# Kernel optimization log

Measured on AMD Instinct MI355X. Metric: run time of the kernel, lower is better.

Reference implementation:

```python
import jax, jax.numpy as jnp
import numpy as np

WIN_SIZE = 256
PATCH_SIZE = [8]
CHANNEL = 32
B_CH = 256        # B_outer(8) * CHANNEL(32)
H, E = 8, 64


def _attn(q, k):
    # q, k: [B*ch, L, H, E] -> softmax scores [B*ch, H, L, L]
    scale = 1.0 / jnp.sqrt(jnp.asarray(E, q.dtype))
    scores = jnp.einsum('blhe,bshe->bhls', q, k) * scale
    return jax.nn.softmax(scores, axis=-1)  # dropout is identity in eval


def _channel_mean(a):
    # '(b reduce_b) l m n -> b l m n' mean with reduce_b=CHANNEL (channel innermost)
    bc, h, m, n = a.shape
    return a.reshape(bc // CHANNEL, CHANNEL, h, m, n).mean(axis=1)


def setup_inputs() -> dict:
    key = jax.random.key(0)
    k1, k2, k3, k4 = jax.random.split(key, 4)
    p = PATCH_SIZE[0]
    patch_num = WIN_SIZE // p
    return {
        'queries_patch_size': jax.random.normal(k1, (B_CH, patch_num, H, E), jnp.float32),
        'keys_patch_size':    jax.random.normal(k2, (B_CH, patch_num, H, E), jnp.float32),
        'queries_patch_num':  jax.random.normal(k3, (B_CH, p, H, E), jnp.float32),
        'keys_patch_num':     jax.random.normal(k4, (B_CH, p, H, E), jnp.float32),
        'patch_index': 0,
        'attn_mask': 0,
    }


def reference(queries_patch_size, keys_patch_size, queries_patch_num, keys_patch_num, patch_index, attn_mask):
    p = PATCH_SIZE[patch_index]
    rep = WIN_SIZE // p

    # patch_size branch: element-wise repeat (einops repeat) then channel mean.
    # mean over channel commutes with the repeat, so reduce first (same math,
    # avoids the 536MB intermediate the torch code materializes).
    s_ps = _channel_mean(_attn(queries_patch_size, keys_patch_size))  # [B,H,rep,rep]
    s_ps = jnp.repeat(jnp.repeat(s_ps, p, axis=2), p, axis=3)

    # patch_num branch: torch .repeat == tile, then channel mean (also commutes).
    s_pn = _channel_mean(_attn(queries_patch_num, keys_patch_num))    # [B,H,p,p]
    s_pn = jnp.tile(s_pn, (1, 1, rep, rep))

    return (s_ps, s_pn)
```

## Files before the change

### kernel.cpp

```cpp
#include <hip/hip_runtime.h>
#include <stdint.h>


__global__ __launch_bounds__(256)
void scores_kernel(const float* __restrict__ qps,
                   const float* __restrict__ kps,
                   const float* __restrict__ qpn,
                   const float* __restrict__ kpn,
                   float* __restrict__ ws_ps,
                   float* __restrict__ ws_pn)
{
    __shared__ float red[4][32 * 36];
    const int tid  = threadIdx.x;
    const int wv   = tid >> 6;
    const int lane = tid & 63;
    const int blk  = blockIdx.x;

    if (blk < 512) {
        const int a     = blk >> 3;
        const int chunk = blk & 7;
        const int bo = a >> 3, h = a & 7;
        const int ch = chunk * 4 + wv;
        const int b  = bo * 32 + ch;
        const int i = lane >> 3, j = lane & 7;

        const float4* Q = reinterpret_cast<const float4*>(qps) + ((b * 32 + 4 * i) * 8 + h) * 16;
        const float4* K = reinterpret_cast<const float4*>(kps) + ((b * 32 + 4 * j) * 8 + h) * 16;

        float acc[4][4];
        #pragma unroll
        for (int r = 0; r < 4; ++r)
            #pragma unroll
            for (int c = 0; c < 4; ++c) acc[r][c] = 0.f;

        #pragma unroll 4
        for (int c = 0; c < 16; ++c) {
            float4 q[4], k[4];
            #pragma unroll
            for (int r = 0; r < 4; ++r) { q[r] = Q[r * 128 + c]; k[r] = K[r * 128 + c]; }
            #pragma unroll
            for (int r = 0; r < 4; ++r)
                #pragma unroll
                for (int u = 0; u < 4; ++u) {
                    acc[r][u] = fmaf(q[r].x, k[u].x, acc[r][u]);
                    acc[r][u] = fmaf(q[r].y, k[u].y, acc[r][u]);
                    acc[r][u] = fmaf(q[r].z, k[u].z, acc[r][u]);
                    acc[r][u] = fmaf(q[r].w, k[u].w, acc[r][u]);
                }
        }

        #pragma unroll
        for (int r = 0; r < 4; ++r) {
            float v0 = acc[r][0] * 0.125f, v1 = acc[r][1] * 0.125f;
            float v2 = acc[r][2] * 0.125f, v3 = acc[r][3] * 0.125f;
            float m = fmaxf(fmaxf(v0, v1), fmaxf(v2, v3));
            m = fmaxf(m, __shfl_xor(m, 1));
            m = fmaxf(m, __shfl_xor(m, 2));
            m = fmaxf(m, __shfl_xor(m, 4));
            float e0 = __expf(v0 - m), e1 = __expf(v1 - m);
            float e2 = __expf(v2 - m), e3 = __expf(v3 - m);
            float s = (e0 + e1) + (e2 + e3);
            s += __shfl_xor(s, 1);
            s += __shfl_xor(s, 2);
            s += __shfl_xor(s, 4);
            const float inv = 1.f / (s * 32.f);
            float4 p; p.x = e0 * inv; p.y = e1 * inv; p.z = e2 * inv; p.w = e3 * inv;
            *reinterpret_cast<float4*>(&red[wv][(4 * i + r) * 36 + 4 * j]) = p;
        }
        __syncthreads();

        const int l = tid >> 3, s4 = (tid & 7) * 4;
        const float4 u0 = *reinterpret_cast<const float4*>(&red[0][l * 36 + s4]);
        const float4 u1 = *reinterpret_cast<const float4*>(&red[1][l * 36 + s4]);
        const float4 u2 = *reinterpret_cast<const float4*>(&red[2][l * 36 + s4]);
        const float4 u3 = *reinterpret_cast<const float4*>(&red[3][l * 36 + s4]);
        float4 o;
        o.x = (u0.x + u1.x) + (u2.x + u3.x);
        o.y = (u0.y + u1.y) + (u2.y + u3.y);
        o.z = (u0.z + u1.z) + (u2.z + u3.z);
        o.w = (u0.w + u1.w) + (u2.w + u3.w);
        reinterpret_cast<float4*>(ws_ps + (a * 8 + chunk) * 1024)[tid] = o;
    } else {
        const int bb    = blk - 512;
        const int a2    = bb >> 3;
        const int chunk = bb & 7;
        const int bo = a2 >> 3, h = a2 & 7;
        const int b  = bo * 32 + chunk * 4 + wv;
        const int i = lane >> 3, j = lane & 7;
        const float4* qv = reinterpret_cast<const float4*>(qpn) + ((b * 8 + i) * 8 + h) * 16;
        const float4* kv = reinterpret_cast<const float4*>(kpn) + ((b * 8 + j) * 8 + h) * 16;

        float acc = 0.f;
        #pragma unroll
        for (int c = 0; c < 16; ++c) {
            float4 q = qv[c], k = kv[c];
            acc = fmaf(q.x, k.x, acc);
            acc = fmaf(q.y, k.y, acc);
            acc = fmaf(q.z, k.z, acc);
            acc = fmaf(q.w, k.w, acc);
        }
        const float s = acc * 0.125f;
        float m = s;
        m = fmaxf(m, __shfl_xor(m, 1));
        m = fmaxf(m, __shfl_xor(m, 2));
        m = fmaxf(m, __shfl_xor(m, 4));
        float e = __expf(s - m);
        float sum = e;
        sum += __shfl_xor(sum, 1);
        sum += __shfl_xor(sum, 2);
        sum += __shfl_xor(sum, 4);

        red[wv][lane] = e / (sum * 32.f);
        __syncthreads();
        if (tid < 64) {
            ws_pn[(a2 * 8 + chunk) * 64 + tid] =
                (red[0][tid] + red[1][tid]) + (red[2][tid] + red[3][tid]);
        }
    }
}

__global__ __launch_bounds__(256)
void reduce_kernel(const float* __restrict__ ws_ps,
                   const float* __restrict__ ws_pn,
                   float* __restrict__ ws0r,
                   float* __restrict__ ws1r)
{
    const int g = blockIdx.x * 256 + threadIdx.x;
    if (g < 65536) {
        const int a = g >> 10, c = g & 1023;
        const float* base = ws_ps + a * 8192 + c;
        float v = 0.f;
        #pragma unroll
        for (int k = 0; k < 8; ++k) v += base[k * 1024];
        ws0r[g] = v;
    } else {
        const int h = g - 65536;
        const int a = h >> 6, c = h & 63;
        const float* base = ws_pn + a * 512 + c;
        float v = 0.f;
        #pragma unroll
        for (int k = 0; k < 8; ++k) v += base[k * 64];
        ws1r[h] = v;
    }
}

__global__ __launch_bounds__(256)
void writer_kernel(const float* __restrict__ ws0r,
                   const float* __restrict__ ws1r,
                   float* __restrict__ out)
{
    const int g = blockIdx.x * 256 + threadIdx.x;
    float4* o4 = reinterpret_cast<float4*>(out);
    if (g < 1048576) {
        const int a  = g >> 14;
        const int r  = g & 16383;
        const int i  = r >> 6;
        const int j4 = r & 63;
        const float v = ws0r[a * 1024 + (i >> 3) * 32 + (j4 >> 1)];
        float4 o; o.x = v; o.y = v; o.z = v; o.w = v;
        o4[g] = o;
    } else {
        const int g2 = g - 1048576;
        const int a  = g2 >> 14;
        const int r  = g2 & 16383;
        const int i  = r >> 6;
        const int j4 = r & 63;
        o4[g] = *reinterpret_cast<const float4*>(ws1r + a * 64 + (i & 7) * 8 + 4 * (j4 & 1));
    }
}

extern "C" void kernel_launch(void* const* d_in, const int* in_sizes, int n_in,
                              void* d_out, int out_size, void* d_ws, size_t ws_size,
                              hipStream_t stream) {
    const float *qps = nullptr, *kps = nullptr, *qpn = nullptr, *kpn = nullptr;
    for (int idx = 0; idx < n_in; ++idx) {
        if (in_sizes[idx] == 256 * 32 * 8 * 64) {
            if (!qps) qps = (const float*)d_in[idx];
            else if (!kps) kps = (const float*)d_in[idx];
        } else if (in_sizes[idx] == 256 * 8 * 8 * 64) {
            if (!qpn) qpn = (const float*)d_in[idx];
            else if (!kpn) kpn = (const float*)d_in[idx];
        }
    }

    float* ws_ps = (float*)d_ws;
    float* ws_pn = ws_ps + 64 * 8 * 1024;
    float* ws0r  = ws_pn + 64 * 8 * 64;
    float* ws1r  = ws0r + 64 * 1024;

    scores_kernel<<<1024, 256, 0, stream>>>(qps, kps, qpn, kpn, ws_ps, ws_pn);
    reduce_kernel<<<272, 256, 0, stream>>>(ws_ps, ws_pn, ws0r, ws1r);
    writer_kernel<<<8192, 256, 0, stream>>>(ws0r, ws1r, (float*)d_out);
}
```

Measured before the change: 118.6 us.

## Stage Q/K tiles in LDS with double buffering and per-thread channel accumulation

The patch_size branch now loads each channel's 32x64 Q and K tiles cooperatively into shared memory with coalesced float4 loads, double-buffered across the block's four channels. Each thread computes one row-group of scores per channel and accumulates the softmax output in registers, which removes the cross-wave LDS reduction. Before, each wave gathered strided global rows and issued redundant global loads across lanes. In exchange, channels inside a block are processed serially with a barrier per channel, and occupancy is pinned through launch_bounds.

Result: faster. 108.8 us (-8.3%).

```diff
diff --git a/kernel.cpp b/kernel.cpp
--- a/kernel.cpp
+++ b/kernel.cpp
@@ -2,7 +2,7 @@
 #include <stdint.h>
 
 
-__global__ __launch_bounds__(256)
+__global__ __launch_bounds__(256, 4)
 void scores_kernel(const float* __restrict__ qps,
                    const float* __restrict__ kps,
                    const float* __restrict__ qpn,
@@ -10,7 +10,7 @@
                    float* __restrict__ ws_ps,
                    float* __restrict__ ws_pn)
 {
-    __shared__ float red[4][32 * 36];
+    __shared__ float4 tiles[2][2][32 * 17];
     const int tid  = threadIdx.x;
     const int wv   = tid >> 6;
     const int lane = tid & 63;
@@ -20,67 +20,94 @@
         const int a     = blk >> 3;
         const int chunk = blk & 7;
         const int bo = a >> 3, h = a & 7;
-        const int ch = chunk * 4 + wv;
-        const int b  = bo * 32 + ch;
-        const int i = lane >> 3, j = lane & 7;
-
-        const float4* Q = reinterpret_cast<const float4*>(qps) + ((b * 32 + 4 * i) * 8 + h) * 16;
-        const float4* K = reinterpret_cast<const float4*>(kps) + ((b * 32 + 4 * j) * 8 + h) * 16;
-
-        float acc[4][4];
-        #pragma unroll
-        for (int r = 0; r < 4; ++r)
+        const int b0 = bo * 32 + chunk * 4;
+
+        const float4* Q4 = reinterpret_cast<const float4*>(qps);
+        const float4* K4 = reinterpret_cast<const float4*>(kps);
+
+        const int r0 = tid >> 4;
+        const int f  = tid & 15;
+
+        const int myrow = wv * 8 + (lane >> 3);
+        const int j     = lane & 7;
+
+        float pa[4];
+        #pragma unroll
+        for (int u = 0; u < 4; ++u) pa[u] = 0.f;
+
+        float4 gq0, gq1, gk0, gk1;
+        {
+            const int b = b0;
+            gq0 = Q4[((b * 32 + r0) * 8 + h) * 16 + f];
+            gq1 = Q4[((b * 32 + 16 + r0) * 8 + h) * 16 + f];
+            gk0 = K4[((b * 32 + r0) * 8 + h) * 16 + f];
+            gk1 = K4[((b * 32 + 16 + r0) * 8 + h) * 16 + f];
+            tiles[0][0][r0 * 17 + f]        = gq0;
+            tiles[0][0][(16 + r0) * 17 + f] = gq1;
+            tiles[0][1][r0 * 17 + f]        = gk0;
+            tiles[0][1][(16 + r0) * 17 + f] = gk1;
+        }
+        __syncthreads();
+
+        for (int ch = 0; ch < 4; ++ch) {
+            const int buf = ch & 1;
+
+            if (ch < 3) {
+                const int b = b0 + ch + 1;
+                gq0 = Q4[((b * 32 + r0) * 8 + h) * 16 + f];
+                gq1 = Q4[((b * 32 + 16 + r0) * 8 + h) * 16 + f];
+                gk0 = K4[((b * 32 + r0) * 8 + h) * 16 + f];
+                gk1 = K4[((b * 32 + 16 + r0) * 8 + h) * 16 + f];
+            }
+
+            float acc[4];
             #pragma unroll
-            for (int c = 0; c < 4; ++c) acc[r][c] = 0.f;
-
-        #pragma unroll 4
-        for (int c = 0; c < 16; ++c) {
-            float4 q[4], k[4];
+            for (int u = 0; u < 4; ++u) acc[u] = 0.f;
             #pragma unroll
-            for (int r = 0; r < 4; ++r) { q[r] = Q[r * 128 + c]; k[r] = K[r * 128 + c]; }
-            #pragma unroll
-            for (int r = 0; r < 4; ++r)
+            for (int c = 0; c < 16; ++c) {
+                const float4 q = tiles[buf][0][myrow * 17 + c];
                 #pragma unroll
                 for (int u = 0; u < 4; ++u) {
-                    acc[r][u] = fmaf(q[r].x, k[u].x, acc[r][u]);
-                    acc[r][u] = fmaf(q[r].y, k[u].y, acc[r][u]);
-                    acc[r][u] = fmaf(q[r].z, k[u].z, acc[r][u]);
-                    acc[r][u] = fmaf(q[r].w, k[u].w, acc[r][u]);
+                    const float4 k = tiles[buf][1][(4 * j + u) * 17 + c];
+                    acc[u] = fmaf(q.x, k.x, acc[u]);
+                    acc[u] = fmaf(q.y, k.y, acc[u]);
+                    acc[u] = fmaf(q.z, k.z, acc[u]);
+                    acc[u] = fmaf(q.w, k.w, acc[u]);
                 }
-        }
-
-        #pragma unroll
-        for (int r = 0; r < 4; ++r) {
-            float v0 = acc[r][0] * 0.125f, v1 = acc[r][1] * 0.125f;
-            float v2 = acc[r][2] * 0.125f, v3 = acc[r][3] * 0.125f;
-            float m = fmaxf(fmaxf(v0, v1), fmaxf(v2, v3));
-            m = fmaxf(m, __shfl_xor(m, 1));
-            m = fmaxf(m, __shfl_xor(m, 2));
-            m = fmaxf(m, __shfl_xor(m, 4));
-            float e0 = __expf(v0 - m), e1 = __expf(v1 - m);
-            float e2 = __expf(v2 - m), e3 = __expf(v3 - m);
-            float s = (e0 + e1) + (e2 + e3);
-            s += __shfl_xor(s, 1);
-            s += __shfl_xor(s, 2);
-            s += __shfl_xor(s, 4);
-            const float inv = 1.f / (s * 32.f);
-            float4 p; p.x = e0 * inv; p.y = e1 * inv; p.z = e2 * inv; p.w = e3 * inv;
-            *reinterpret_cast<float4*>(&red[wv][(4 * i + r) * 36 + 4 * j]) = p;
-        }
-        __syncthreads();
-
-        const int l = tid >> 3, s4 = (tid & 7) * 4;
-        const float4 u0 = *reinterpret_cast<const float4*>(&red[0][l * 36 + s4]);
-        const float4 u1 = *reinterpret_cast<const float4*>(&red[1][l * 36 + s4]);
-        const float4 u2 = *reinterpret_cast<const float4*>(&red[2][l * 36 + s4]);
-        const float4 u3 = *reinterpret_cast<const float4*>(&red[3][l * 36 + s4]);
-        float4 o;
-        o.x = (u0.x + u1.x) + (u2.x + u3.x);
-        o.y = (u0.y + u1.y) + (u2.y + u3.y);
-        o.z = (u0.z + u1.z) + (u2.z + u3.z);
-        o.w = (u0.w + u1.w) + (u2.w + u3.w);
-        reinterpret_cast<float4*>(ws_ps + (a * 8 + chunk) * 1024)[tid] = o;
+            }
+
+            {
+                float v0 = acc[0] * 0.125f, v1 = acc[1] * 0.125f;
+                float v2 = acc[2] * 0.125f, v3 = acc[3] * 0.125f;
+                float m = fmaxf(fmaxf(v0, v1), fmaxf(v2, v3));
+                m = fmaxf(m, __shfl_xor(m, 1));
+                m = fmaxf(m, __shfl_xor(m, 2));
+                m = fmaxf(m, __shfl_xor(m, 4));
+                float e0 = __expf(v0 - m), e1 = __expf(v1 - m);
+                float e2 = __expf(v2 - m), e3 = __expf(v3 - m);
+                float s = (e0 + e1) + (e2 + e3);
+                s += __shfl_xor(s, 1);
+                s += __shfl_xor(s, 2);
+                s += __shfl_xor(s, 4);
+                const float inv = 1.f / (s * 32.f);
+                pa[0] += e0 * inv; pa[1] += e1 * inv;
+                pa[2] += e2 * inv; pa[3] += e3 * inv;
+            }
+
+            if (ch < 3) {
+                const int nb = buf ^ 1;
+                tiles[nb][0][r0 * 17 + f]        = gq0;
+                tiles[nb][0][(16 + r0) * 17 + f] = gq1;
+                tiles[nb][1][r0 * 17 + f]        = gk0;
+                tiles[nb][1][(16 + r0) * 17 + f] = gk1;
+            }
+            __syncthreads();
+        }
+
+        float4 o; o.x = pa[0]; o.y = pa[1]; o.z = pa[2]; o.w = pa[3];
+        reinterpret_cast<float4*>(ws_ps + (a * 8 + chunk) * 1024)[myrow * 8 + j] = o;
     } else {
+        float* red = reinterpret_cast<float*>(tiles);
         const int bb    = blk - 512;
         const int a2    = bb >> 3;
         const int chunk = bb & 7;
@@ -110,11 +137,12 @@
         sum += __shfl_xor(sum, 2);
         sum += __shfl_xor(sum, 4);
 
-        red[wv][lane] = e / (sum * 32.f);
+        red[wv * 64 + lane] = e / (sum * 32.f);
         __syncthreads();
         if (tid < 64) {
             ws_pn[(a2 * 8 + chunk) * 64 + tid] =
-                (red[0][tid] + red[1][tid]) + (red[2][tid] + red[3][tid]);
+                (red[0 * 64 + tid] + red[1 * 64 + tid]) +
+                (red[2 * 64 + tid] + red[3 * 64 + tid]);
         }
     }
 }
```
